# Performance work log

Hardware: AMD Instinct MI355X
Metric: run time of the kernel (lower is better)

The kernel has to match this reference:

```python
import jax, jax.numpy as jnp
import numpy as np

DIM = 2048
DIM_HEADS = 64
NUM_HEADS = DIM // DIM_HEADS  # 32


def setup_inputs() -> dict:
    key = jax.random.key(0)
    k1, k2, k3, k4 = jax.random.split(key, 4)
    B, N = 2, 2048
    x = jax.random.normal(k1, (B, N, DIM), dtype=jnp.float32)
    freqs = jax.random.normal(k2, (N, DIM_HEADS), dtype=jnp.float32)
    W_qkv = jax.random.normal(k3, (3 * DIM, DIM), dtype=jnp.float32) * 0.02
    W_out = jax.random.normal(k4, (DIM, DIM), dtype=jnp.float32) * 0.02
    return {"x": x, "freqs": freqs, "W_qkv": W_qkv, "W_out": W_out}


def _rotate_half(x):
    # split last dim into two halves (j=2), return cat(-x2, x1)
    x1, x2 = jnp.split(x, 2, axis=-1)
    return jnp.concatenate([-x2, x1], axis=-1)


def _apply_rotary_pos_emb(t, freqs, scale=1.0):
    # t: [b, h, n, d]; freqs: [n, rot_dim]; rotary math in float32
    out_dtype = t.dtype
    rot_dim = freqs.shape[-1]
    seq_len = t.shape[-2]
    freqs = freqs.astype(jnp.float32)[-seq_len:, :]  # [n, rot_dim]
    t = t.astype(jnp.float32)
    t_rot, t_unrot = t[..., :rot_dim], t[..., rot_dim:]
    t_rot = t_rot * jnp.cos(freqs) * scale + _rotate_half(t_rot) * jnp.sin(freqs) * scale
    return jnp.concatenate([t_rot.astype(out_dtype), t_unrot.astype(out_dtype)], axis=-1)


def reference(x, freqs, W_qkv, W_out):
    B, N, _ = x.shape
    h, d = NUM_HEADS, DIM_HEADS
    # fused QKV projection (Linear, no bias): x @ W_qkv.T
    qkv = jnp.einsum('bnc,fc->bnf', x, W_qkv)  # [B, N, 3*DIM]
    q, k, v = jnp.split(qkv, 3, axis=-1)
    q = q.reshape(B, N, h, d).transpose(0, 2, 1, 3)  # [B, h, N, d]
    k = k.reshape(B, N, h, d).transpose(0, 2, 1, 3)
    v = v.reshape(B, N, h, d).transpose(0, 2, 1, 3)
    # equal q/k seq lens -> ratio = 1, same freqs for both
    q = _apply_rotary_pos_emb(q, freqs)
    k = _apply_rotary_pos_emb(k, freqs)
    # scaled dot-product attention (non-causal)
    scale = 1.0 / np.sqrt(d).astype(np.float32)
    scores = jnp.einsum('bhqd,bhkd->bhqk', q, k) * scale
    attn = jax.nn.softmax(scores, axis=-1)
    out = jnp.einsum('bhqk,bhkd->bhqd', attn, v)
    out = out.transpose(0, 2, 1, 3).reshape(B, N, h * d)  # [B, N, DIM]
    return jnp.einsum('bnc,oc->bno', out, W_out)
```

## Files before the change

kernel.cpp:

```cpp
#include <hip/hip_runtime.h>

#define DIMC 2048
#define NSEQ 2048
#define NBATCH 2
#define NH 32
#define DH 64
#define BHEADS (NBATCH*NH)
#define MROWS (NBATCH*NSEQ)
#define NQKV (3*DIMC)

typedef __attribute__((ext_vector_type(8))) short short8;
typedef __attribute__((ext_vector_type(4))) float f32x4;
typedef __attribute__((ext_vector_type(4))) unsigned int uint4v;
typedef __attribute__((ext_vector_type(2))) unsigned int u32x2;

static __device__ __forceinline__ unsigned short f2bf(float f) {
  union { float f; unsigned int u; } v; v.f = f;
  unsigned int r = (v.u + 0x7FFFu + ((v.u >> 16) & 1u)) >> 16;
  return (unsigned short)r;
}

static __device__ __forceinline__ unsigned int cvt_pk_bf16(float lo, float hi) {
  unsigned int r;
  asm("v_cvt_pk_bf16_f32 %0, %1, %2" : "=v"(r) : "v"(lo), "v"(hi));
  return r;
}

#define BAR()    __builtin_amdgcn_s_barrier()
#define FENCE()  asm volatile("" ::: "memory")
#define LGKM0()  asm volatile("s_waitcnt lgkmcnt(0)" ::: "memory")
#define VM(n)    asm volatile("s_waitcnt vmcnt(" #n ")" ::: "memory")

__global__ __launch_bounds__(256) void cvt_bf16(const float* __restrict__ in,
                                                unsigned short* __restrict__ out,
                                                int n8) {
  int i = blockIdx.x * blockDim.x + threadIdx.x;
  int stride = gridDim.x * blockDim.x;
  for (; i < n8; i += stride) {
    const float4* p = (const float4*)in + (size_t)i * 2;
    float4 a = p[0], b = p[1];
    union { unsigned short u[8]; uint4v v; } o;
    o.u[0] = f2bf(a.x); o.u[1] = f2bf(a.y); o.u[2] = f2bf(a.z); o.u[3] = f2bf(a.w);
    o.u[4] = f2bf(b.x); o.u[5] = f2bf(b.y); o.u[6] = f2bf(b.z); o.u[7] = f2bf(b.w);
    *((uint4v*)out + i) = o.v;
  }
}

__global__ __launch_bounds__(256) void build_cs(const float* __restrict__ freqs,
                                                float2* __restrict__ cs, int n) {
  int i = blockIdx.x * blockDim.x + threadIdx.x;
  if (i < n) { float f = freqs[i]; cs[i] = make_float2(cosf(f), sinf(f)); }
}

#define QSCALE 0.18033688011112042f
#define SLOT 24576

template<int EPI>
__global__ __launch_bounds__(512, 1) void gemm128(
    const unsigned short* __restrict__ A,
    const unsigned short* __restrict__ Bm,
    int Kdim, int Ncols,
    float* __restrict__ Cout,
    unsigned short* __restrict__ qo, unsigned short* __restrict__ ko,
    unsigned short* __restrict__ vo, const float2* __restrict__ cs)
{
  extern __shared__ char Lds[];
  const int t = threadIdx.x;
  const int w = t >> 6, lane = t & 63, lr = lane & 15, g = lane >> 4;
  const int wm = w >> 2, wn = w & 3;
  const int gxs = (g * 16) ^ (((lr >> 1) & 3) << 4);

  const int nx = gridDim.x;
  int orig = blockIdx.y * nx + blockIdx.x;
  int cpx = (nx * gridDim.y) >> 3;
  int id = (orig & 7) * cpx + (orig >> 3);
  const int m0 = (id / nx) * 128;
  const int n0 = (id % nx) * 256;

  const int rowt = t >> 2;
  const int colt = ((t & 3) ^ ((t >> 3) & 3)) * 8;
  const unsigned short* Abase = A + (size_t)(m0 + rowt) * Kdim + colt;
  const unsigned short* Bbase = Bm + (size_t)(n0 + rowt) * Kdim + colt;
  char* dstw = Lds + w * 1024;

  auto STAGE = [&](int sbuf, int T) {
    const unsigned short* sa = Abase + T * 32;
    const unsigned short* sb = Bbase + T * 32;
    __builtin_amdgcn_global_load_lds(
        (const __attribute__((address_space(1))) void*)sa,
        (__attribute__((address_space(3))) void*)(dstw + sbuf), 16, 0, 0);
    __builtin_amdgcn_global_load_lds(
        (const __attribute__((address_space(1))) void*)sb,
        (__attribute__((address_space(3))) void*)(dstw + sbuf + 8192), 16, 0, 0);
    __builtin_amdgcn_global_load_lds(
        (const __attribute__((address_space(1))) void*)(sb + (size_t)128 * Kdim),
        (__attribute__((address_space(3))) void*)(dstw + sbuf + 16384), 16, 0, 0);
  };

  short8 Af[4], Bf[4];
  auto LDAB = [&](int rb) {
    const char* ap = Lds + rb + (wm * 64 + lr) * 64 + gxs;
    const char* bp = Lds + rb + 8192 + (wn * 64 + lr) * 64 + gxs;
    #pragma unroll
    for (int m = 0; m < 4; m++) Af[m] = *(const short8*)(ap + m * 1024);
    #pragma unroll
    for (int n = 0; n < 4; n++) Bf[n] = *(const short8*)(bp + n * 1024);
  };

  f32x4 acc[4][4];
  f32x4 zero = {0.0f, 0.0f, 0.0f, 0.0f};
  #pragma unroll
  for (int i = 0; i < 4; i++)
    #pragma unroll
    for (int j = 0; j < 4; j++) acc[i][j] = zero;

  STAGE(0, 0); STAGE(SLOT, 1);
  VM(3);
  BAR(); FENCE();

  const int NT = Kdim >> 5;
  int rb = 0, sb = 2 * SLOT;
  for (int i = 0; i < NT; i++) {
    LDAB(rb);
    if (i + 2 < NT) STAGE(sb, i + 2);
    BAR(); LGKM0();
    __builtin_amdgcn_s_setprio(1);
    #pragma unroll
    for (int m = 0; m < 4; m++)
      #pragma unroll
      for (int n = 0; n < 4; n++)
        acc[m][n] = __builtin_amdgcn_mfma_f32_16x16x32_bf16(Af[m], Bf[n], acc[m][n], 0, 0, 0);
    __builtin_amdgcn_s_setprio(0);
    if (i < NT - 2) { VM(3); } else { VM(0); }
    BAR(); FENCE();
    rb += SLOT; if (rb == 3 * SLOT) rb = 0;
    sb += SLOT; if (sb == 3 * SLOT) sb = 0;
  }

  if (EPI == 0) {
    #pragma unroll
    for (int m = 0; m < 4; m++) {
      #pragma unroll
      for (int r = 0; r < 4; r++) {
        int row = m0 + wm * 64 + m * 16 + g * 4 + r;
        #pragma unroll
        for (int n = 0; n < 4; n++)
          Cout[(size_t)row * Ncols + (n0 + wn * 64 + n * 16 + lr)] = acc[m][n][r];
      }
    }
  } else {
    const int which = n0 >> 11;
    const int head = ((n0 & 2047) + wn * 64) >> 6;
    #pragma unroll
    for (int m = 0; m < 4; m++) {
      #pragma unroll
      for (int r = 0; r < 4; r++) {
        int row = m0 + wm * 64 + m * 16 + g * 4 + r;
        int b = row >> 11, ntok = row & 2047;
        size_t obase = ((size_t)(b * NH + head) * NSEQ + ntok) * DH;
        #pragma unroll
        for (int n = 0; n < 4; n++) {
          int d = n * 16 + lr;
          float val = acc[m][n][r];
          if (which == 2) {
            vo[obase + d] = f2bf(val);
          } else {
            float other = acc[m][n ^ 2][r];
            float2 c2 = cs[ntok * DH + d];
            float rot = (d < 32) ? (val * c2.x - other * c2.y)
                                 : (val * c2.x + other * c2.y);
            if (which == 0) qo[obase + d] = f2bf(rot * QSCALE);
            else            ko[obase + d] = f2bf(rot);
          }
        }
      }
    }
  }
}

__global__ __launch_bounds__(256, 4) void attn_fa(
    const unsigned short* __restrict__ qb,
    const unsigned short* __restrict__ kb,
    const unsigned short* __restrict__ vb,
    unsigned short* __restrict__ aob)
{
  __shared__ __align__(16) unsigned short Kl[64 * 64];
  __shared__ __align__(16) unsigned short Vt[64 * 72];
  __shared__ __align__(16) unsigned short Pl[4][32 * 76];

  const int t = threadIdx.x;
  const int w = t >> 6, lane = t & 63, lr = lane & 15, g = lane >> 4;
  const int bh = blockIdx.y;
  const int q0 = blockIdx.x * 128 + w * 32;
  const size_t hbase = (size_t)bh * NSEQ * DH;

  short8 qf[2][2];
  #pragma unroll
  for (int qt = 0; qt < 2; qt++)
    #pragma unroll
    for (int hf = 0; hf < 2; hf++)
      qf[qt][hf] = *(const short8*)(qb + hbase + (size_t)(q0 + qt * 16 + lr) * DH + hf * 32 + g * 8);

  f32x4 zero = {0.0f, 0.0f, 0.0f, 0.0f};
  f32x4 oacc[2][4];
  #pragma unroll
  for (int qt = 0; qt < 2; qt++)
    #pragma unroll
    for (int dv = 0; dv < 4; dv++) oacc[qt][dv] = zero;
  float mrun[2] = {-1e30f, -1e30f};
  float lrun[2] = {0.0f, 0.0f};

  int kro[2], kdo_[2];
  #pragma unroll
  for (int c = 0; c < 2; c++) {
    int b = w * 2048 + c * 1024 + lane * 16;
    int row = b >> 7;
    int off = b ^ ((row & 7) << 4);
    kro[c] = row;
    kdo_[c] = (off >> 1) & 63;
  }
  const int vr0 = (t & 31) * 2;
  const int vhv = (t >> 5) * 8;

  unsigned short* prow0 = &Pl[w][lr * 76];
  unsigned short* prow1 = &Pl[w][(16 + lr) * 76];

  for (int kv0 = 0; kv0 < NSEQ; kv0 += 64) {
    __syncthreads();
    #pragma unroll
    for (int c = 0; c < 2; c++) {
      const unsigned short* src = kb + hbase + (size_t)(kv0 + kro[c]) * DH + kdo_[c];
      __builtin_amdgcn_global_load_lds(
          (const __attribute__((address_space(1))) void*)src,
          (__attribute__((address_space(3))) void*)(Kl + w * 1024 + c * 512), 16, 0, 0);
    }
    {
      const unsigned short* s0 = vb + hbase + (size_t)(kv0 + vr0) * DH + vhv;
      short8 v0 = *(const short8*)(s0);
      short8 v1 = *(const short8*)(s0 + DH);
      #pragma unroll
      for (int j = 0; j < 8; j++) {
        unsigned int p = ((unsigned short)v0[j]) | (((unsigned int)(unsigned short)v1[j]) << 16);
        *(unsigned int*)&Vt[(vhv + j) * 72 + vr0] = p;
      }
    }
    __syncthreads();

    f32x4 s[2][4];
    #pragma unroll
    for (int kt = 0; kt < 4; kt++) {
      int row = kt * 16 + lr;
      int sw = (row & 7) << 4;
      int byteA = (row * 128 + g * 16) ^ sw;
      int byteB = (row * 128 + 64 + g * 16) ^ sw;
      short8 kA = *(const short8*)((const char*)Kl + byteA);
      short8 kB = *(const short8*)((const char*)Kl + byteB);
      #pragma unroll
      for (int qt = 0; qt < 2; qt++) {
        f32x4 a0 = __builtin_amdgcn_mfma_f32_16x16x32_bf16(kA, qf[qt][0], zero, 0, 0, 0);
        s[qt][kt] = __builtin_amdgcn_mfma_f32_16x16x32_bf16(kB, qf[qt][1], a0, 0, 0, 0);
      }
    }

    float nm[2];
    #pragma unroll
    for (int qt = 0; qt < 2; qt++) {
      f32x4 m01 = s[qt][0];
      #pragma unroll
      for (int kt = 1; kt < 4; kt++) {
        f32x4 sv = s[qt][kt];
        m01[0] = fmaxf(m01[0], sv[0]); m01[1] = fmaxf(m01[1], sv[1]);
        m01[2] = fmaxf(m01[2], sv[2]); m01[3] = fmaxf(m01[3], sv[3]);
      }
      float v = fmaxf(fmaxf(m01[0], m01[1]), fmaxf(m01[2], m01[3]));
      v = fmaxf(v, __shfl_xor(v, 16));
      v = fmaxf(v, __shfl_xor(v, 32));
      nm[qt] = v;
    }

    if (!__all(fmaxf(nm[0] - mrun[0], nm[1] - mrun[1]) <= 8.0f)) {
      const int sb = (lane & 48) + ((lane & 48) >> 2);
      #pragma unroll
      for (int qt = 0; qt < 2; qt++) {
        float m2 = fmaxf(mrun[qt], nm[qt]);
        float cc = exp2f(mrun[qt] - m2);
        mrun[qt] = m2;
        lrun[qt] *= cc;
        float c0r = __shfl(cc, sb + 0);
        float c1r = __shfl(cc, sb + 1);
        float c2r = __shfl(cc, sb + 2);
        float c3r = __shfl(cc, sb + 3);
        #pragma unroll
        for (int dv = 0; dv < 4; dv++) {
          f32x4 a = oacc[qt][dv];
          a[0] *= c0r; a[1] *= c1r; a[2] *= c2r; a[3] *= c3r;
          oacc[qt][dv] = a;
        }
      }
    }

    #pragma unroll
    for (int qt = 0; qt < 2; qt++) {
      float mq = mrun[qt];
      float ls = 0.0f;
      unsigned short* prow = qt ? prow1 : prow0;
      #pragma unroll
      for (int kt = 0; kt < 4; kt++) {
        f32x4 sv = s[qt][kt];
        float p0 = exp2f(sv[0] - mq), p1 = exp2f(sv[1] - mq);
        float p2 = exp2f(sv[2] - mq), p3 = exp2f(sv[3] - mq);
        ls += (p0 + p1) + (p2 + p3);
        u32x2 uu;
        uu.x = cvt_pk_bf16(p0, p1);
        uu.y = cvt_pk_bf16(p2, p3);
        *(u32x2*)(prow + kt * 16 + g * 4) = uu;
      }
      ls += __shfl_xor(ls, 16);
      ls += __shfl_xor(ls, 32);
      lrun[qt] += ls;
    }

    #pragma unroll
    for (int c0 = 0; c0 < 2; c0++) {
      short8 pa0 = *(const short8*)(prow0 + c0 * 32 + g * 8);
      short8 pa1 = *(const short8*)(prow1 + c0 * 32 + g * 8);
      #pragma unroll
      for (int dv = 0; dv < 4; dv++) {
        short8 vf = *(const short8*)&Vt[(dv * 16 + lr) * 72 + c0 * 32 + g * 8];
        oacc[0][dv] = __builtin_amdgcn_mfma_f32_16x16x32_bf16(pa0, vf, oacc[0][dv], 0, 0, 0);
        oacc[1][dv] = __builtin_amdgcn_mfma_f32_16x16x32_bf16(pa1, vf, oacc[1][dv], 0, 0, 0);
      }
    }
  }

  const int b = bh >> 5, h = bh & 31;
  const int sb = (lane & 48) + ((lane & 48) >> 2);
  #pragma unroll
  for (int qt = 0; qt < 2; qt++) {
    float inv = 1.0f / lrun[qt];
    float ir[4];
    ir[0] = __shfl(inv, sb + 0);
    ir[1] = __shfl(inv, sb + 1);
    ir[2] = __shfl(inv, sb + 2);
    ir[3] = __shfl(inv, sb + 3);
    #pragma unroll
    for (int r = 0; r < 4; r++) {
      int ntok = q0 + qt * 16 + g * 4 + r;
      size_t ob = ((size_t)(b * NSEQ + ntok)) * DIMC + h * DH;
      #pragma unroll
      for (int dv = 0; dv < 4; dv++)
        aob[ob + dv * 16 + lr] = f2bf(oacc[qt][dv][r] * ir[r]);
    }
  }
}

extern "C" void kernel_launch(void* const* d_in, const int* in_sizes, int n_in,
                              void* d_out, int out_size, void* d_ws, size_t ws_size,
                              hipStream_t stream) {
  const float* x     = (const float*)d_in[0];
  const float* freqs = (const float*)d_in[1];
  const float* Wqkv  = (const float*)d_in[2];
  const float* Wout  = (const float*)d_in[3];
  float* out = (float*)d_out;

  char* ws = (char*)d_ws;
  size_t off = 0;
  auto alloc = [&](size_t bytes) {
    void* p = ws + off;
    off += (bytes + 255) & ~(size_t)255;
    return p;
  };
  unsigned short* xb    = (unsigned short*)alloc((size_t)MROWS * DIMC * 2);
  unsigned short* wqkvb = (unsigned short*)alloc((size_t)NQKV * DIMC * 2);
  unsigned short* woutb = (unsigned short*)alloc((size_t)DIMC * DIMC * 2);
  unsigned short* qbuf  = (unsigned short*)alloc((size_t)BHEADS * NSEQ * DH * 2);
  unsigned short* kbuf  = (unsigned short*)alloc((size_t)BHEADS * NSEQ * DH * 2);
  unsigned short* vbuf  = (unsigned short*)alloc((size_t)BHEADS * NSEQ * DH * 2);
  float2* cst           = (float2*)alloc((size_t)NSEQ * DH * sizeof(float2));
  unsigned short* aob   = xb;

  (void)hipFuncSetAttribute((const void*)gemm128<1>,
      hipFuncAttributeMaxDynamicSharedMemorySize, 3 * SLOT);
  (void)hipFuncSetAttribute((const void*)gemm128<0>,
      hipFuncAttributeMaxDynamicSharedMemorySize, 3 * SLOT);

  cvt_bf16<<<2048, 256, 0, stream>>>(x, xb, MROWS * DIMC / 8);
  cvt_bf16<<<2048, 256, 0, stream>>>(Wqkv, wqkvb, NQKV * DIMC / 8);
  cvt_bf16<<<1024, 256, 0, stream>>>(Wout, woutb, DIMC * DIMC / 8);
  build_cs<<<(NSEQ * DH + 255) / 256, 256, 0, stream>>>(freqs, cst, NSEQ * DH);

  gemm128<1><<<dim3(NQKV / 256, MROWS / 128), 512, 3 * SLOT, stream>>>(
      xb, wqkvb, DIMC, NQKV, nullptr, qbuf, kbuf, vbuf, cst);

  attn_fa<<<dim3(NSEQ / 128, BHEADS), 256, 0, stream>>>(qbuf, kbuf, vbuf, aob);

  gemm128<0><<<dim3(DIMC / 256, MROWS / 128), 512, 3 * SLOT, stream>>>(
      aob, woutb, DIMC, DIMC, out, nullptr, nullptr, nullptr, nullptr);
}
```

Baseline: 355.5 us.

## Double-buffer K/V tiles in flash attention and use raw v_exp_f32

The attention kernel now double-buffers the K and V shared-memory tiles. It issues the global loads for the next 64-key chunk before computing on the current one, and uses one barrier per iteration instead of two. The exp2f calls become a raw v_exp_f32, which drops the library's range handling, and MFMA blocks are wrapped in s_setprio to favour matrix issue. The extra LDS lowers the occupancy hint from 4 to 3 blocks per CU, and the P row padding changes from 76 to 72, which may change bank conflicts.

```diff
diff --git a/kernel.cpp b/kernel.cpp
--- a/kernel.cpp
+++ b/kernel.cpp
@@ -23,6 +23,12 @@
 static __device__ __forceinline__ unsigned int cvt_pk_bf16(float lo, float hi) {
   unsigned int r;
   asm("v_cvt_pk_bf16_f32 %0, %1, %2" : "=v"(r) : "v"(lo), "v"(hi));
+  return r;
+}
+
+static __device__ __forceinline__ float fexp2(float x) {
+  float r;
+  asm("v_exp_f32 %0, %1" : "=v"(r) : "v"(x));
   return r;
 }
 
@@ -178,15 +184,15 @@
   }
 }
 
-__global__ __launch_bounds__(256, 4) void attn_fa(
+__global__ __launch_bounds__(256, 3) void attn_fa(
     const unsigned short* __restrict__ qb,
     const unsigned short* __restrict__ kb,
     const unsigned short* __restrict__ vb,
     unsigned short* __restrict__ aob)
 {
-  __shared__ __align__(16) unsigned short Kl[64 * 64];
-  __shared__ __align__(16) unsigned short Vt[64 * 72];
-  __shared__ __align__(16) unsigned short Pl[4][32 * 76];
+  __shared__ __align__(16) unsigned short Kl[2][64 * 64];
+  __shared__ __align__(16) unsigned short Vt[2][64 * 72];
+  __shared__ __align__(16) unsigned short Pl[4][32 * 72];
 
   const int t = threadIdx.x;
   const int w = t >> 6, lane = t & 63, lr = lane & 15, g = lane >> 4;
@@ -222,29 +228,53 @@
   const int vr0 = (t & 31) * 2;
   const int vhv = (t >> 5) * 8;
 
-  unsigned short* prow0 = &Pl[w][lr * 76];
-  unsigned short* prow1 = &Pl[w][(16 + lr) * 76];
-
-  for (int kv0 = 0; kv0 < NSEQ; kv0 += 64) {
-    __syncthreads();
+  unsigned short* prow0 = &Pl[w][lr * 72];
+  unsigned short* prow1 = &Pl[w][(16 + lr) * 72];
+
+  auto STAGE_K = [&](int buf, int kv0) {
     #pragma unroll
     for (int c = 0; c < 2; c++) {
       const unsigned short* src = kb + hbase + (size_t)(kv0 + kro[c]) * DH + kdo_[c];
       __builtin_amdgcn_global_load_lds(
           (const __attribute__((address_space(1))) void*)src,
-          (__attribute__((address_space(3))) void*)(Kl + w * 1024 + c * 512), 16, 0, 0);
-    }
-    {
-      const unsigned short* s0 = vb + hbase + (size_t)(kv0 + vr0) * DH + vhv;
-      short8 v0 = *(const short8*)(s0);
-      short8 v1 = *(const short8*)(s0 + DH);
-      #pragma unroll
-      for (int j = 0; j < 8; j++) {
-        unsigned int p = ((unsigned short)v0[j]) | (((unsigned int)(unsigned short)v1[j]) << 16);
-        *(unsigned int*)&Vt[(vhv + j) * 72 + vr0] = p;
-      }
-    }
-    __syncthreads();
+          (__attribute__((address_space(3))) void*)(&Kl[buf][0] + w * 1024 + c * 512), 16, 0, 0);
+    }
+  };
+  auto LOAD_V = [&](int kv0, short8& v0, short8& v1) {
+    const unsigned short* s0 = vb + hbase + (size_t)(kv0 + vr0) * DH + vhv;
+    v0 = *(const short8*)(s0);
+    v1 = *(const short8*)(s0 + DH);
+  };
+  auto WRITE_V = [&](int buf, short8 v0, short8 v1) {
+    #pragma unroll
+    for (int j = 0; j < 8; j++) {
+      unsigned int p = ((unsigned short)v0[j]) | (((unsigned int)(unsigned short)v1[j]) << 16);
+      *(unsigned int*)&Vt[buf][(vhv + j) * 72 + vr0] = p;
+    }
+  };
+
+  {
+    short8 pv0, pv1;
+    STAGE_K(0, 0);
+    LOAD_V(0, pv0, pv1);
+    VM(0);
+    WRITE_V(0, pv0, pv1);
+    LGKM0();
+    BAR(); FENCE();
+  }
+
+  const int NC = NSEQ / 64;
+  for (int it = 0; it < NC; it++) {
+    const int cur = it & 1;
+    const bool more = (it + 1 < NC);
+    short8 nv0, nv1;
+    if (more) {
+      STAGE_K(cur ^ 1, (it + 1) * 64);
+      LOAD_V((it + 1) * 64, nv0, nv1);
+    }
+
+    const char* Kb = (const char*)&Kl[cur][0];
+    const unsigned short* Vb = &Vt[cur][0];
 
     f32x4 s[2][4];
     #pragma unroll
@@ -253,13 +283,15 @@
       int sw = (row & 7) << 4;
       int byteA = (row * 128 + g * 16) ^ sw;
       int byteB = (row * 128 + 64 + g * 16) ^ sw;
-      short8 kA = *(const short8*)((const char*)Kl + byteA);
-      short8 kB = *(const short8*)((const char*)Kl + byteB);
+      short8 kA = *(const short8*)(Kb + byteA);
+      short8 kB = *(const short8*)(Kb + byteB);
+      __builtin_amdgcn_s_setprio(1);
       #pragma unroll
       for (int qt = 0; qt < 2; qt++) {
         f32x4 a0 = __builtin_amdgcn_mfma_f32_16x16x32_bf16(kA, qf[qt][0], zero, 0, 0, 0);
         s[qt][kt] = __builtin_amdgcn_mfma_f32_16x16x32_bf16(kB, qf[qt][1], a0, 0, 0, 0);
       }
+      __builtin_amdgcn_s_setprio(0);
     }
 
     float nm[2];
@@ -283,7 +315,7 @@
       #pragma unroll
       for (int qt = 0; qt < 2; qt++) {
         float m2 = fmaxf(mrun[qt], nm[qt]);
-        float cc = exp2f(mrun[qt] - m2);
+        float cc = fexp2(mrun[qt] - m2);
         mrun[qt] = m2;
         lrun[qt] *= cc;
         float c0r = __shfl(cc, sb + 0);
@@ -307,8 +339,8 @@
       #pragma unroll
       for (int kt = 0; kt < 4; kt++) {
         f32x4 sv = s[qt][kt];
-        float p0 = exp2f(sv[0] - mq), p1 = exp2f(sv[1] - mq);
-        float p2 = exp2f(sv[2] - mq), p3 = exp2f(sv[3] - mq);
+        float p0 = fexp2(sv[0] - mq), p1 = fexp2(sv[1] - mq);
+        float p2 = fexp2(sv[2] - mq), p3 = fexp2(sv[3] - mq);
         ls += (p0 + p1) + (p2 + p3);
         u32x2 uu;
         uu.x = cvt_pk_bf16(p0, p1);
@@ -324,13 +356,22 @@
     for (int c0 = 0; c0 < 2; c0++) {
       short8 pa0 = *(const short8*)(prow0 + c0 * 32 + g * 8);
       short8 pa1 = *(const short8*)(prow1 + c0 * 32 + g * 8);
+      __builtin_amdgcn_s_setprio(1);
       #pragma unroll
       for (int dv = 0; dv < 4; dv++) {
-        short8 vf = *(const short8*)&Vt[(dv * 16 + lr) * 72 + c0 * 32 + g * 8];
+        short8 vf = *(const short8*)&Vb[(dv * 16 + lr) * 72 + c0 * 32 + g * 8];
         oacc[0][dv] = __builtin_amdgcn_mfma_f32_16x16x32_bf16(pa0, vf, oacc[0][dv], 0, 0, 0);
         oacc[1][dv] = __builtin_amdgcn_mfma_f32_16x16x32_bf16(pa1, vf, oacc[1][dv], 0, 0, 0);
       }
-    }
+      __builtin_amdgcn_s_setprio(0);
+    }
+
+    if (more) {
+      VM(0);
+      WRITE_V(cur ^ 1, nv0, nv1);
+    }
+    LGKM0();
+    BAR(); FENCE();
   }
 
   const int b = bh >> 5, h = bh & 31;
```

After: 323.5 us. -9.0%, faster.
